# Kernel tuning notes

Hardware: AMD Instinct MI355X
Metric: run time of the kernel (lower is better)

The kernel has to match this reference:

```python
import jax, jax.numpy as jnp
import numpy as np

B, D, H, N, M, TOPK = 8, 128, 4, 2048, 2048, 32
DH = D // H  # per-head dim = 32
BN_EPS = 1e-5


def _conv1(W, b, z):
    # Conv1d kernel_size=1: [out,in] x [b,in,n] -> [b,out,n]
    return jnp.einsum('oc,bcn->bon', W, z) + b[None, :, None]


def setup_inputs() -> dict:
    key = jax.random.key(0)
    ks = jax.random.split(key, 20)
    s = 1.0 / np.sqrt(D)
    s2 = 1.0 / np.sqrt(2 * D)
    return {
        'x': jax.random.normal(ks[0], (B, D, N), jnp.float32),
        'source': jax.random.normal(ks[1], (B, D, M), jnp.float32),
        'Wq': jax.random.normal(ks[2], (D, D), jnp.float32) * s,
        'bq': jax.random.normal(ks[3], (D,), jnp.float32) * 0.01,
        'Wk': jax.random.normal(ks[4], (D, D), jnp.float32) * s,
        'bk': jax.random.normal(ks[5], (D,), jnp.float32) * 0.01,
        'Wv': jax.random.normal(ks[6], (D, D), jnp.float32) * s,
        'bv': jax.random.normal(ks[7], (D,), jnp.float32) * 0.01,
        'Wm': jax.random.normal(ks[8], (D, D), jnp.float32) * s,
        'bm': jax.random.normal(ks[9], (D,), jnp.float32) * 0.01,
        'W1': jax.random.normal(ks[10], (2 * D, 2 * D), jnp.float32) * s2,
        'b1': jax.random.normal(ks[11], (2 * D,), jnp.float32) * 0.01,
        'g1': jnp.ones((2 * D,), jnp.float32),
        'beta1': jnp.zeros((2 * D,), jnp.float32),
        'mu1': jax.random.normal(ks[12], (2 * D,), jnp.float32) * 0.1,
        'var1': jax.random.uniform(ks[13], (2 * D,), jnp.float32, 0.5, 1.5),
        'W2': jax.random.normal(ks[14], (D, 2 * D), jnp.float32) * s2,
        'b2': jnp.zeros((D,), jnp.float32),  # nn.init.constant_(mlp[-1].bias, 0)
        'k': TOPK,
    }


def reference(x, source, Wq, bq, Wk, bk, Wv, bv, Wm, bm,
              W1, b1, g1, beta1, mu1, var1, W2, b2, k):
    b, d, n = x.shape
    m = source.shape[2]
    h, dh = H, d // H
    # projections; torch .view(b, dim, heads, -1) splits channel dim row-major
    q = _conv1(Wq, bq, x).reshape(b, dh, h, n)
    kk = _conv1(Wk, bk, source).reshape(b, dh, h, m)
    v = _conv1(Wv, bv, source).reshape(b, dh, h, m)
    # dynamic_attention3: dense scores, topk, sparse softmax, scatter
    scores = jnp.einsum('bdhn,bdhm->bhnm', q, kk) / np.sqrt(dh)  # [b,h,n,m]
    topv, topi = jax.lax.top_k(scores, k)                        # [b,h,n,k]
    S = jax.nn.softmax(topv, axis=-1)
    bi = jnp.arange(b)[:, None, None, None]
    hi = jnp.arange(h)[None, :, None, None]
    ni = jnp.arange(n)[None, None, :, None]
    prob = jnp.zeros((b, h, n, m), scores.dtype).at[bi, hi, ni, topi].set(S)
    msg = jnp.einsum('bhnm,bdhm->bdhn', prob, v).reshape(b, d, n)
    msg = _conv1(Wm, bm, msg)  # merge
    # AttentionalPropagation MLP([2d, 2d, d]) with BN+ReLU (inference BN)
    cat = jnp.concatenate([x, msg], axis=1)  # [b,2d,n]
    z = _conv1(W1, b1, cat)
    z = (z - mu1[None, :, None]) * jax.lax.rsqrt(var1 + BN_EPS)[None, :, None]
    z = z * g1[None, :, None] + beta1[None, :, None]
    z = jax.nn.relu(z)
    delta = _conv1(W2, b2, z)  # [b,d,n]
    return delta
```

## Files before the change

kernel.cpp:

```cpp
#include <hip/hip_runtime.h>

#define BB   8
#define DD   128
#define HHH  4
#define NNN  2048
#define MMM  2048
#define DH   32
#define TN   8
#define SCPAD 34
#define SCROWS (64 * SCPAD)

typedef float v2f __attribute__((ext_vector_type(2)));

template<int MODE>
__global__ __launch_bounds__(256)
void gemm_k(const float* __restrict__ W, const float* __restrict__ bias,
            const float* __restrict__ X0, const float* __restrict__ X1,
            float* __restrict__ out, int K, int Mrows,
            const float* __restrict__ g1, const float* __restrict__ be1,
            const float* __restrict__ mu1, const float* __restrict__ va1)
{
  __shared__ float Wt[32][132];
  __shared__ float Xl[32][64];
  const int tid = threadIdx.x;
  const int b   = blockIdx.x >> 5;
  const int n0  = (blockIdx.x & 31) << 6;
  const int rblk = blockIdx.y << 7;
  const int tx = tid & 15, ty = tid >> 4;

  float acc[8][4];
#pragma unroll
  for (int i = 0; i < 8; ++i)
#pragma unroll
    for (int j = 0; j < 4; ++j) acc[i][j] = 0.f;

  for (int k0 = 0; k0 < K; k0 += 32) {
#pragma unroll
    for (int i = 0; i < 4; ++i) {
      int idx = tid + i * 256;
      int r = idx >> 3, kv = (idx & 7) << 2;
      const float4 w4 = *(const float4*)&W[(size_t)(rblk + r) * K + k0 + kv];
      Wt[kv + 0][r] = w4.x; Wt[kv + 1][r] = w4.y;
      Wt[kv + 2][r] = w4.z; Wt[kv + 3][r] = w4.w;
    }
#pragma unroll
    for (int i = 0; i < 2; ++i) {
      int idx = tid + i * 256;
      int kk = idx >> 4, j4 = (idx & 15) << 2;
      int kg = k0 + kk;
      const float* src;
      if (MODE == 2)
        src = (kg < DD) ? &X0[((size_t)b * DD + kg) * NNN]
                        : &X1[((size_t)b * DD + (kg - DD)) * NNN];
      else
        src = &X0[((size_t)b * K + kg) * NNN];
      *(float4*)&Xl[kk][j4] = *(const float4*)&src[n0 + j4];
    }
    __syncthreads();
#pragma unroll
    for (int kk = 0; kk < 32; ++kk) {
      float a[8], bx[4];
      *(float4*)&a[0] = *(const float4*)&Wt[kk][ty * 8];
      *(float4*)&a[4] = *(const float4*)&Wt[kk][ty * 8 + 4];
      *(float4*)&bx[0] = *(const float4*)&Xl[kk][tx * 4];
#pragma unroll
      for (int i = 0; i < 8; ++i)
#pragma unroll
        for (int j = 0; j < 4; ++j) acc[i][j] = fmaf(a[i], bx[j], acc[i][j]);
    }
    __syncthreads();
  }

#pragma unroll
  for (int i = 0; i < 8; ++i) {
    const int r = rblk + ty * 8 + i;
    const float bv = bias[r];
    float scale = 1.f, shift = 0.f;
    if (MODE == 2) {
      const float inv = rsqrtf(va1[r] + 1e-5f);
      scale = g1[r] * inv;
      shift = be1[r] - mu1[r] * scale;
    }
#pragma unroll
    for (int j = 0; j < 4; ++j) {
      const int n = n0 + tx * 4 + j;
      float v = acc[i][j] + bv;
      if (MODE == 2) { v = fmaf(v, scale, shift); v = v > 0.f ? v : 0.f; }
      if (MODE == 0) {
        out[(((size_t)b * HHH + (r & 3)) * NNN + n) * DH + (r >> 2)] = v;
      } else {
        out[((size_t)b * Mrows + r) * NNN + n] = v;
      }
    }
  }
}

__device__ __forceinline__ void pk_fma(v2f& acc, v2f a, v2f b) {
  asm("v_pk_fma_f32 %0, %1, %2, %0" : "+v"(acc) : "v"(a), "v"(b));
}

__device__ __forceinline__ int dpp_scan_i32(int v) {
  v += __builtin_amdgcn_update_dpp(0, v, 0x111, 0xF, 0xF, true);
  v += __builtin_amdgcn_update_dpp(0, v, 0x112, 0xF, 0xF, true);
  v += __builtin_amdgcn_update_dpp(0, v, 0x114, 0xF, 0xF, true);
  v += __builtin_amdgcn_update_dpp(0, v, 0x118, 0xF, 0xF, true);
  v += __builtin_amdgcn_update_dpp(0, v, 0x142, 0xA, 0xF, true);
  v += __builtin_amdgcn_update_dpp(0, v, 0x143, 0xC, 0xF, true);
  return v;
}

__device__ __forceinline__ float dpp_sum_f32(float v) {
  float t;
#define DPPSTEP(ctrl, rm)                                                     \
  t = __uint_as_float((unsigned)__builtin_amdgcn_update_dpp(                  \
          0, (int)__float_as_uint(v), ctrl, rm, 0xF, true));                  \
  v += t;
  DPPSTEP(0x111, 0xF) DPPSTEP(0x112, 0xF) DPPSTEP(0x114, 0xF)
  DPPSTEP(0x118, 0xF) DPPSTEP(0x142, 0xA) DPPSTEP(0x143, 0xC)
#undef DPPSTEP
  return v;
}

__device__ __forceinline__ unsigned ordkey(float f) {
  unsigned b = __float_as_uint(f);
  return (b & 0x80000000u) ? ~b : (b | 0x80000000u);
}

__device__ __forceinline__ void transpose32(unsigned (&A)[32]) {
  unsigned m = 0x0000FFFFu;
#pragma unroll
  for (int j = 16; j != 0; j = j >> 1, m = m ^ (m << j)) {
#pragma unroll
    for (int k = 0; k < 32; ++k) {
      if (!(k & j)) {
        unsigned t = (A[k] ^ (A[k + j] >> j)) & m;
        A[k]     ^= t;
        A[k + j] ^= t << j;
      }
    }
  }
}

__global__ __launch_bounds__(256, 2)
void attn_k(const float* __restrict__ qt, const float* __restrict__ kt,
            const float* __restrict__ vt, float* __restrict__ msg)
{
  extern __shared__ char smem[];
  float* Sc = (float*)smem;
  float (*Kl)[36] = (float(*)[36])(smem + (size_t)TN * SCROWS * 4);

  const int tid  = threadIdx.x;
  const int wave = tid >> 6, lane = tid & 63;
  const int h = blockIdx.y, b = blockIdx.z;
  const int n0 = blockIdx.x * TN;
  const size_t bh = (size_t)b * HHH + h;
  const float* kbase = kt + bh * MMM * DH;
  const float* vbase = vt + bh * MMM * DH;
  const float* qbase = qt + (bh * NNN + n0) * DH;

  v2f q0p[16], q1p[16];
  {
    const float4* qr0 = (const float4*)(qbase + (size_t)(wave * 2 + 0) * DH);
    const float4* qr1 = (const float4*)(qbase + (size_t)(wave * 2 + 1) * DH);
#pragma unroll
    for (int i = 0; i < 8; ++i) {
      const float4 t0 = qr0[i], t1 = qr1[i];
      q0p[2*i].x = t0.x; q0p[2*i].y = t0.y;
      q0p[2*i+1].x = t0.z; q0p[2*i+1].y = t0.w;
      q1p[2*i].x = t1.x; q1p[2*i].y = t1.y;
      q1p[2*i+1].x = t1.z; q1p[2*i+1].y = t1.w;
    }
  }

  float* s0 = Sc + (size_t)(wave * 2 + 0) * SCROWS + lane * SCPAD;
  float* s1 = Sc + (size_t)(wave * 2 + 1) * SCROWS + lane * SCPAD;

  const float4* kg4 = (const float4*)kbase;
  const int m0 = tid >> 3, e0 = (tid & 7) << 2;

  auto chunk = [&](int c, float4& f0, float4& f1) {
    __syncthreads();
    *(float4*)&Kl[m0][e0]      = f0;
    *(float4*)&Kl[m0 + 32][e0] = f1;
    if (c + 2 < 32) {
      f0 = kg4[(c + 2) * 512 + tid];
      f1 = kg4[(c + 2) * 512 + tid + 256];
    }
    __syncthreads();
    v2f acc0; acc0.x = 0.f; acc0.y = 0.f;
    v2f acc1; acc1.x = 0.f; acc1.y = 0.f;
#pragma unroll
    for (int i = 0; i < 8; ++i) {
      const float4 kv4 = *(const float4*)&Kl[lane][i * 4];
      v2f k01; k01.x = kv4.x; k01.y = kv4.y;
      v2f k23; k23.x = kv4.z; k23.y = kv4.w;
      pk_fma(acc0, q0p[2*i],   k01);
      pk_fma(acc0, q0p[2*i+1], k23);
      pk_fma(acc1, q1p[2*i],   k01);
      pk_fma(acc1, q1p[2*i+1], k23);
    }
    s0[c] = acc0.x + acc0.y;
    s1[c] = acc1.x + acc1.y;
  };

  float4 pA0 = kg4[tid],       pA1 = kg4[tid + 256];
  float4 pB0 = kg4[512 + tid], pB1 = kg4[512 + tid + 256];
  for (int c = 0; c < 32; c += 2) {
    chunk(c,     pA0, pA1);
    chunk(c + 1, pB0, pB1);
  }
  __syncthreads();

  unsigned A0[32], A1[32];
#pragma unroll
  for (int i = 0; i < 16; ++i) {
    const float2 v0 = *(const float2*)&s0[2 * i];
    const float2 v1 = *(const float2*)&s1[2 * i];
    A0[31 - 2 * i]     = ordkey(v0.x);
    A0[31 - 2 * i - 1] = ordkey(v0.y);
    A1[31 - 2 * i]     = ordkey(v1.x);
    A1[31 - 2 * i - 1] = ordkey(v1.y);
  }
  transpose32(A0);
  transpose32(A1);

  unsigned act0 = ~0u, act1 = ~0u, def0 = 0u, def1 = 0u, tau0 = 0u, tau1 = 0u;
  int Kq0 = 32, Kq1 = 32, rem0 = MMM, rem1 = MMM;
  bool done0 = false, done1 = false;

#pragma unroll
  for (int g = 0; g < 4; ++g) {
    if (!(done0 && done1)) {
#pragma unroll
      for (int ii = 0; ii < 8; ++ii) {
        const int i = g * 8 + ii;
        const unsigned h0 = act0 & A0[i];
        const unsigned h1 = act1 & A1[i];
        int pk = __builtin_popcount(h0) | (__builtin_popcount(h1) << 16);
        pk = dpp_scan_i32(pk);
        const int s = __builtin_amdgcn_readlane(pk, 63);
        const int c0 = s & 0xFFFF, c1 = (int)((unsigned)s >> 16);
        if (!done0) {
          if (c0 >= Kq0) { act0 = h0; tau0 |= 1u << (31 - i); rem0 = c0; }
          else { Kq0 -= c0; def0 |= h0; act0 &= ~A0[i]; rem0 -= c0; }
          done0 = (rem0 == Kq0);
        }
        if (!done1) {
          if (c1 >= Kq1) { act1 = h1; tau1 |= 1u << (31 - i); rem1 = c1; }
          else { Kq1 -= c1; def1 |= h1; act1 &= ~A1[i]; rem1 -= c1; }
          done1 = (rem1 == Kq1);
        }
      }
    }
  }

  float* scrP = (float*)&Kl[0][0] + wave * 64;
  int*   scrM = (int*)(scrP + 32);
  const int e = lane & 31, half = lane >> 5;
  const float rs = 0.17677669529663687f;

#pragma unroll
  for (int r = 0; r < 2; ++r) {
    unsigned a_r = (r == 0) ? act0 : act1;
    const bool done_r = (r == 0) ? done0 : done1;
    const int  Kq_r   = (r == 0) ? Kq0 : Kq1;
    if (!done_r) {
      unsigned sact = 0u;
      int remq = Kq_r;
      for (int j = 0; j < 32 && remq > 0; ++j) {
        const unsigned long long bal = __ballot((a_r >> j) & 1u);
        const int cnt = __popcll(bal);
        const int take = cnt < remq ? cnt : remq;
        const unsigned long long below = bal & ((1ull << lane) - 1ull);
        if (((a_r >> j) & 1u) && (int)__popcll(below) < take)
          sact |= 1u << j;
        remq -= take;
      }
      a_r = sact;
    }
    const unsigned sel = ((r == 0) ? def0 : def1) | a_r;
    const unsigned tau_r = (r == 0) ? tau0 : tau1;
    const unsigned tb = (tau_r & 0x80000000u) ? (tau_r & 0x7FFFFFFFu) : ~tau_r;
    const float tauf = __uint_as_float(tb);
    const float* srow = (r == 0) ? s0 : s1;

    const int ns = __builtin_popcount(sel);
    int pos = dpp_scan_i32(ns) - ns;
    asm volatile("s_waitcnt lgkmcnt(0)" ::: "memory");
    unsigned mrem = sel;
    while (mrem) {
      const int j = __ffs(mrem) - 1; mrem &= mrem - 1;
      scrP[pos] = __expf((srow[j] - tauf) * rs);
      scrM[pos] = j * 64 + lane;
      ++pos;
    }
    asm volatile("s_waitcnt lgkmcnt(0)" ::: "memory");

    const float pmine = (lane < 32) ? scrP[lane] : 0.f;
    const float tot = __uint_as_float(
        __builtin_amdgcn_readlane(__float_as_uint(dpp_sum_f32(pmine)), 63));
    const float rinv = 1.0f / tot;

    float accv = 0.f;
#pragma unroll
    for (int jj = 0; jj < 16; ++jj) {
      const int j2 = jj * 2 + half;
      const float pj = scrP[j2];
      const int   mj = scrM[j2];
      accv = fmaf(pj, vbase[(size_t)mj * DH + e], accv);
    }
    accv += __shfl_xor(accv, 32);
    accv *= rinv;
    if (lane < 32)
      msg[((size_t)b * DD + (e * HHH + h)) * NNN + (n0 + wave * 2 + r)] = accv;
  }
}

extern "C" void kernel_launch(void* const* d_in, const int* in_sizes, int n_in,
                              void* d_out, int out_size, void* d_ws, size_t ws_size,
                              hipStream_t stream)
{
  const float* x   = (const float*)d_in[0];
  const float* src = (const float*)d_in[1];
  const float* Wq  = (const float*)d_in[2];
  const float* bq  = (const float*)d_in[3];
  const float* Wk  = (const float*)d_in[4];
  const float* bk  = (const float*)d_in[5];
  const float* Wv  = (const float*)d_in[6];
  const float* bv  = (const float*)d_in[7];
  const float* Wm  = (const float*)d_in[8];
  const float* bm  = (const float*)d_in[9];
  const float* W1  = (const float*)d_in[10];
  const float* b1  = (const float*)d_in[11];
  const float* g1  = (const float*)d_in[12];
  const float* be1 = (const float*)d_in[13];
  const float* mu1 = (const float*)d_in[14];
  const float* va1 = (const float*)d_in[15];
  const float* W2  = (const float*)d_in[16];
  const float* b2  = (const float*)d_in[17];

  float* ws = (float*)d_ws;
  const size_t SEG = 2097152;
  float* q_t  = ws;
  float* k_t  = ws + SEG;
  float* v_t  = ws + 2 * SEG;
  float* msg  = ws + 3 * SEG;
  float* msg2 = ws;
  float* z    = ws + SEG;

  const dim3 blk(256);
  const dim3 g128(256, 1), g256(256, 2);

  gemm_k<0><<<g128, blk, 0, stream>>>(Wq, bq, x,   nullptr, q_t, 128, 128,
                                      nullptr, nullptr, nullptr, nullptr);
  gemm_k<0><<<g128, blk, 0, stream>>>(Wk, bk, src, nullptr, k_t, 128, 128,
                                      nullptr, nullptr, nullptr, nullptr);
  gemm_k<0><<<g128, blk, 0, stream>>>(Wv, bv, src, nullptr, v_t, 128, 128,
                                      nullptr, nullptr, nullptr, nullptr);

  const size_t smem = (size_t)TN * SCROWS * 4 + 64 * 36 * 4;
  hipFuncSetAttribute(reinterpret_cast<const void*>(attn_k),
                      hipFuncAttributeMaxDynamicSharedMemorySize, (int)smem);
  const dim3 ga(NNN / TN, HHH, BB);
  attn_k<<<ga, blk, smem, stream>>>(q_t, k_t, v_t, msg);

  gemm_k<1><<<g128, blk, 0, stream>>>(Wm, bm, msg, nullptr, msg2, 128, 128,
                                      nullptr, nullptr, nullptr, nullptr);
  gemm_k<2><<<g256, blk, 0, stream>>>(W1, b1, x, msg2, z, 256, 256,
                                      g1, be1, mu1, va1);
  gemm_k<3><<<g128, blk, 0, stream>>>(W2, b2, z, nullptr, (float*)d_out, 256, 128,
                                      nullptr, nullptr, nullptr, nullptr);
}
```

Before: 451.7 us.

## Compute attention scores with bf16x3 split MFMA instead of packed FP32 FMA

The QK^T score computation in the attention kernel moves from v_pk_fma_f32 to 16x16x32 bf16 MFMA. Q and K are split into three bf16 parts (hi/mid/lo) and six cross products are summed, keeping near-FP32 accuracy for the top-k selection. The block grows to 512 threads covering 16 queries, and K tiles of 128 keys are staged in LDS as bf16 planes. The intent is to cut the FMA-bound score phase. The cost is larger LDS use for scores and extra split/pack work, and any residual rounding could change which keys land in the top-k near ties.

Measured after the change: 462.4 us. 2.4% more time.

```diff
diff --git a/kernel.cpp b/kernel.cpp
--- a/kernel.cpp
+++ b/kernel.cpp
@@ -6,11 +6,10 @@
 #define NNN  2048
 #define MMM  2048
 #define DH   32
-#define TN   8
-#define SCPAD 34
-#define SCROWS (64 * SCPAD)
-
-typedef float v2f __attribute__((ext_vector_type(2)));
+#define TN   16
+
+typedef __attribute__((ext_vector_type(8))) short   s8b;
+typedef __attribute__((ext_vector_type(4))) float   f32x4;
 
 template<int MODE>
 __global__ __launch_bounds__(256)
@@ -95,10 +94,6 @@
   }
 }
 
-__device__ __forceinline__ void pk_fma(v2f& acc, v2f a, v2f b) {
-  asm("v_pk_fma_f32 %0, %1, %2, %0" : "+v"(acc) : "v"(a), "v"(b));
-}
-
 __device__ __forceinline__ int dpp_scan_i32(int v) {
   v += __builtin_amdgcn_update_dpp(0, v, 0x111, 0xF, 0xF, true);
   v += __builtin_amdgcn_update_dpp(0, v, 0x112, 0xF, 0xF, true);
@@ -141,13 +136,26 @@
   }
 }
 
-__global__ __launch_bounds__(256, 2)
+__device__ __forceinline__ unsigned pk2(float a, float b, float& ra, float& rb) {
+  const unsigned ua = __float_as_uint(a), ub = __float_as_uint(b);
+  ra = a - __uint_as_float(ua & 0xFFFF0000u);
+  rb = b - __uint_as_float(ub & 0xFFFF0000u);
+  return (ua >> 16) | (ub & 0xFFFF0000u);
+}
+__device__ __forceinline__ unsigned pk2f(float a, float b) {
+  return (__float_as_uint(a) >> 16) | (__float_as_uint(b) & 0xFFFF0000u);
+}
+
+__global__ __launch_bounds__(512, 2)
 void attn_k(const float* __restrict__ qt, const float* __restrict__ kt,
             const float* __restrict__ vt, float* __restrict__ msg)
 {
   extern __shared__ char smem[];
   float* Sc = (float*)smem;
-  float (*Kl)[36] = (float(*)[36])(smem + (size_t)TN * SCROWS * 4);
+  char*  KB = smem + (size_t)TN * 2048 * 4;
+  char*  KH = KB;
+  char*  KM = KB + 8192;
+  char*  KL = KB + 16384;
 
   const int tid  = threadIdx.x;
   const int wave = tid >> 6, lane = tid & 63;
@@ -158,68 +166,78 @@
   const float* vbase = vt + bh * MMM * DH;
   const float* qbase = qt + (bh * NNN + n0) * DH;
 
-  v2f q0p[16], q1p[16];
+  s8b ah, am, al;
   {
-    const float4* qr0 = (const float4*)(qbase + (size_t)(wave * 2 + 0) * DH);
-    const float4* qr1 = (const float4*)(qbase + (size_t)(wave * 2 + 1) * DH);
-#pragma unroll
-    for (int i = 0; i < 8; ++i) {
-      const float4 t0 = qr0[i], t1 = qr1[i];
-      q0p[2*i].x = t0.x; q0p[2*i].y = t0.y;
-      q0p[2*i+1].x = t0.z; q0p[2*i+1].y = t0.w;
-      q1p[2*i].x = t1.x; q1p[2*i].y = t1.y;
-      q1p[2*i+1].x = t1.z; q1p[2*i+1].y = t1.w;
-    }
-  }
-
-  float* s0 = Sc + (size_t)(wave * 2 + 0) * SCROWS + lane * SCPAD;
-  float* s1 = Sc + (size_t)(wave * 2 + 1) * SCROWS + lane * SCPAD;
+    const float* qr = qbase + (size_t)(lane & 15) * DH + (lane >> 4) * 8;
+    const float4 f0 = *(const float4*)qr;
+    const float4 f1 = *(const float4*)(qr + 4);
+    float r0, r1, r2, r3, r4, r5, r6, r7;
+    float t0, t1, t2, t3, t4, t5, t6, t7;
+    int4 H, M, L;
+    H.x = pk2(f0.x, f0.y, r0, r1);  H.y = pk2(f0.z, f0.w, r2, r3);
+    H.z = pk2(f1.x, f1.y, r4, r5);  H.w = pk2(f1.z, f1.w, r6, r7);
+    M.x = pk2(r0, r1, t0, t1);      M.y = pk2(r2, r3, t2, t3);
+    M.z = pk2(r4, r5, t4, t5);      M.w = pk2(r6, r7, t6, t7);
+    L.x = pk2f(t0, t1);             L.y = pk2f(t2, t3);
+    L.z = pk2f(t4, t5);             L.w = pk2f(t6, t7);
+    ah = *(s8b*)&H; am = *(s8b*)&M; al = *(s8b*)&L;
+  }
+
+  const int mst   = tid >> 3;
+  const int best0 = mst * 64 + (tid & 7) * 8;
+  const int best1 = best0 + 64 * 64;
+
+  const int boff = (wave * 16 + (lane & 15)) * 64 + (lane >> 4) * 16;
 
   const float4* kg4 = (const float4*)kbase;
-  const int m0 = tid >> 3, e0 = (tid & 7) << 2;
-
-  auto chunk = [&](int c, float4& f0, float4& f1) {
+  float4 p0 = kg4[tid], p1 = kg4[tid + 512];
+  const f32x4 Z = {0.f, 0.f, 0.f, 0.f};
+
+  for (int c = 0; c < 16; ++c) {
+    uint2 H0, M0, L0, H1, M1, L1;
+    {
+      float r0, r1, r2, r3, t0, t1, t2, t3;
+      H0.x = pk2(p0.x, p0.y, r0, r1); H0.y = pk2(p0.z, p0.w, r2, r3);
+      M0.x = pk2(r0, r1, t0, t1);     M0.y = pk2(r2, r3, t2, t3);
+      L0.x = pk2f(t0, t1);            L0.y = pk2f(t2, t3);
+      H1.x = pk2(p1.x, p1.y, r0, r1); H1.y = pk2(p1.z, p1.w, r2, r3);
+      M1.x = pk2(r0, r1, t0, t1);     M1.y = pk2(r2, r3, t2, t3);
+      L1.x = pk2f(t0, t1);            L1.y = pk2f(t2, t3);
+    }
     __syncthreads();
-    *(float4*)&Kl[m0][e0]      = f0;
-    *(float4*)&Kl[m0 + 32][e0] = f1;
-    if (c + 2 < 32) {
-      f0 = kg4[(c + 2) * 512 + tid];
-      f1 = kg4[(c + 2) * 512 + tid + 256];
-    }
+    *(uint2*)(KH + best0) = H0;  *(uint2*)(KH + best1) = H1;
+    *(uint2*)(KM + best0) = M0;  *(uint2*)(KM + best1) = M1;
+    *(uint2*)(KL + best0) = L0;  *(uint2*)(KL + best1) = L1;
     __syncthreads();
-    v2f acc0; acc0.x = 0.f; acc0.y = 0.f;
-    v2f acc1; acc1.x = 0.f; acc1.y = 0.f;
-#pragma unroll
-    for (int i = 0; i < 8; ++i) {
-      const float4 kv4 = *(const float4*)&Kl[lane][i * 4];
-      v2f k01; k01.x = kv4.x; k01.y = kv4.y;
-      v2f k23; k23.x = kv4.z; k23.y = kv4.w;
-      pk_fma(acc0, q0p[2*i],   k01);
-      pk_fma(acc0, q0p[2*i+1], k23);
-      pk_fma(acc1, q1p[2*i],   k01);
-      pk_fma(acc1, q1p[2*i+1], k23);
-    }
-    s0[c] = acc0.x + acc0.y;
-    s1[c] = acc1.x + acc1.y;
-  };
-
-  float4 pA0 = kg4[tid],       pA1 = kg4[tid + 256];
-  float4 pB0 = kg4[512 + tid], pB1 = kg4[512 + tid + 256];
-  for (int c = 0; c < 32; c += 2) {
-    chunk(c,     pA0, pA1);
-    chunk(c + 1, pB0, pB1);
+    if (c < 15) {
+      p0 = kg4[(c + 1) * 1024 + tid];
+      p1 = kg4[(c + 1) * 1024 + tid + 512];
+    }
+    const s8b bhf = *(const s8b*)(KH + boff);
+    const s8b bmf = *(const s8b*)(KM + boff);
+    const s8b blf = *(const s8b*)(KL + boff);
+    f32x4 a1 = __builtin_amdgcn_mfma_f32_16x16x32_bf16(ah, bhf, Z, 0, 0, 0);
+    f32x4 a2 = __builtin_amdgcn_mfma_f32_16x16x32_bf16(ah, bmf, Z, 0, 0, 0);
+    a1 = __builtin_amdgcn_mfma_f32_16x16x32_bf16(am, bhf, a1, 0, 0, 0);
+    a2 = __builtin_amdgcn_mfma_f32_16x16x32_bf16(am, bmf, a2, 0, 0, 0);
+    a1 = __builtin_amdgcn_mfma_f32_16x16x32_bf16(ah, blf, a1, 0, 0, 0);
+    a2 = __builtin_amdgcn_mfma_f32_16x16x32_bf16(al, bhf, a2, 0, 0, 0);
+    const int mglob = c * 128 + wave * 16 + (lane & 15);
+    const int rbase = (lane >> 4) * 4;
+#pragma unroll
+    for (int j = 0; j < 4; ++j)
+      Sc[(size_t)(rbase + j) * 2048 + mglob] = a1[j] + a2[j];
   }
   __syncthreads();
 
+  const float* sA = Sc + (size_t)(2 * wave + 0) * 2048 + lane;
+  const float* sB = Sc + (size_t)(2 * wave + 1) * 2048 + lane;
+
   unsigned A0[32], A1[32];
 #pragma unroll
-  for (int i = 0; i < 16; ++i) {
-    const float2 v0 = *(const float2*)&s0[2 * i];
-    const float2 v1 = *(const float2*)&s1[2 * i];
-    A0[31 - 2 * i]     = ordkey(v0.x);
-    A0[31 - 2 * i - 1] = ordkey(v0.y);
-    A1[31 - 2 * i]     = ordkey(v1.x);
-    A1[31 - 2 * i - 1] = ordkey(v1.y);
+  for (int j = 0; j < 32; ++j) {
+    A0[31 - j] = ordkey(sA[j * 64]);
+    A1[31 - j] = ordkey(sB[j * 64]);
   }
   transpose32(A0);
   transpose32(A1);
@@ -254,7 +272,7 @@
     }
   }
 
-  float* scrP = (float*)&Kl[0][0] + wave * 64;
+  float* scrP = (float*)KB + wave * 64;
   int*   scrM = (int*)(scrP + 32);
   const int e = lane & 31, half = lane >> 5;
   const float rs = 0.17677669529663687f;
@@ -282,7 +300,7 @@
     const unsigned tau_r = (r == 0) ? tau0 : tau1;
     const unsigned tb = (tau_r & 0x80000000u) ? (tau_r & 0x7FFFFFFFu) : ~tau_r;
     const float tauf = __uint_as_float(tb);
-    const float* srow = (r == 0) ? s0 : s1;
+    const float* srow = (r == 0) ? sA : sB;
 
     const int ns = __builtin_popcount(sel);
     int pos = dpp_scan_i32(ns) - ns;
@@ -290,7 +308,7 @@
     unsigned mrem = sel;
     while (mrem) {
       const int j = __ffs(mrem) - 1; mrem &= mrem - 1;
-      scrP[pos] = __expf((srow[j] - tauf) * rs);
+      scrP[pos] = __expf((srow[j * 64] - tauf) * rs);
       scrM[pos] = j * 64 + lane;
       ++pos;
     }
@@ -312,7 +330,7 @@
     accv += __shfl_xor(accv, 32);
     accv *= rinv;
     if (lane < 32)
-      msg[((size_t)b * DD + (e * HHH + h)) * NNN + (n0 + wave * 2 + r)] = accv;
+      msg[((size_t)b * DD + (e * HHH + h)) * NNN + (n0 + 2 * wave + r)] = accv;
   }
 }
 
@@ -358,11 +376,11 @@
   gemm_k<0><<<g128, blk, 0, stream>>>(Wv, bv, src, nullptr, v_t, 128, 128,
                                       nullptr, nullptr, nullptr, nullptr);
 
-  const size_t smem = (size_t)TN * SCROWS * 4 + 64 * 36 * 4;
+  const size_t smem = (size_t)TN * 2048 * 4 + 3 * 128 * 32 * 2;
   hipFuncSetAttribute(reinterpret_cast<const void*>(attn_k),
                       hipFuncAttributeMaxDynamicSharedMemorySize, (int)smem);
   const dim3 ga(NNN / TN, HHH, BB);
-  attn_k<<<ga, blk, smem, stream>>>(q_t, k_t, v_t, msg);
+  attn_k<<<ga, dim3(512), smem, stream>>>(q_t, k_t, v_t, msg);
 
   gemm_k<1><<<g128, blk, 0, stream>>>(Wm, bm, msg, nullptr, msg2, 128, 128,
                                       nullptr, nullptr, nullptr, nullptr);
```
